# Kernel tuning notes

Measured on AMD Instinct MI355X. Metric: run time of the kernel, lower is better.

## Reference

```python
import jax, jax.numpy as jnp
import numpy as np

D_MODEL = 512
PROJ = 2 * D_MODEL  # 1024
N_STATES = 32
KSIZE = 4
LN_EPS = 1e-3  # keras LayerNormalization default epsilon


def setup_inputs() -> dict:
    key = jax.random.key(0)
    ks = jax.random.split(key, 16)
    B, L = 2, 2048
    s_in = 1.0 / np.sqrt(D_MODEL)
    s_pr = 1.0 / np.sqrt(PROJ)
    x = jax.random.normal(ks[0], (B, L, D_MODEL), dtype=jnp.float32)
    # LayerNorm params
    ln_gamma = jnp.ones((D_MODEL,), jnp.float32)
    ln_beta = jnp.zeros((D_MODEL,), jnp.float32)
    # dense1 / dense2: d_model -> proj
    W1 = jax.random.normal(ks[1], (D_MODEL, PROJ), jnp.float32) * s_in
    b1 = jnp.zeros((PROJ,), jnp.float32)
    W2 = jax.random.normal(ks[2], (D_MODEL, PROJ), jnp.float32) * s_in
    b2 = jnp.zeros((PROJ,), jnp.float32)
    # depthwise causal conv1d: kernel (K, 1, PROJ) in WIO layout, groups=PROJ
    conv_k = jax.random.normal(ks[3], (KSIZE, 1, PROJ), jnp.float32) * 0.5
    conv_b = jnp.zeros((PROJ,), jnp.float32)
    # SSM params
    A_log = jnp.log(jnp.broadcast_to(jnp.arange(1, N_STATES + 1, dtype=jnp.float32), (PROJ, N_STATES)))
    D_skip = jnp.ones((PROJ,), jnp.float32)
    WB = jax.random.normal(ks[4], (PROJ, N_STATES), jnp.float32) * s_pr
    bB = jnp.zeros((N_STATES,), jnp.float32)
    WC = jax.random.normal(ks[5], (PROJ, N_STATES), jnp.float32) * s_pr
    bC = jnp.zeros((N_STATES,), jnp.float32)
    Wd = jax.random.normal(ks[6], (PROJ, PROJ), jnp.float32) * s_pr
    bd = jnp.zeros((PROJ,), jnp.float32)
    # dense3: proj -> d_model
    W3 = jax.random.normal(ks[7], (PROJ, D_MODEL), jnp.float32) * s_pr
    b3 = jnp.zeros((D_MODEL,), jnp.float32)
    return dict(x=x, ln_gamma=ln_gamma, ln_beta=ln_beta, W1=W1, b1=b1, W2=W2, b2=b2,
                conv_k=conv_k, conv_b=conv_b, A_log=A_log, D_skip=D_skip,
                WB=WB, bB=bB, WC=WC, bC=bC, Wd=Wd, bd=bd, W3=W3, b3=b3)


def _layernorm(x, gamma, beta):
    mu = jnp.mean(x, axis=-1, keepdims=True)
    var = jnp.mean(jnp.square(x - mu), axis=-1, keepdims=True)
    return (x - mu) * jax.lax.rsqrt(var + LN_EPS) * gamma + beta


def _causal_dwconv(x, k, b):
    # x: [B,L,C], k: [K,1,C], depthwise causal conv (left-pad K-1)
    y = jax.lax.conv_general_dilated(
        x, k, window_strides=(1,), padding=[(KSIZE - 1, 0)],
        dimension_numbers=('NWC', 'WIO', 'NWC'), feature_group_count=PROJ)
    return y + b


def _selective_scan(u, delta, A, Bm, Cm, D_skip):
    # u, delta: [B,L,D]; A: [D,N]; Bm, Cm: [B,L,N]; D_skip: [D]
    deltaA = jnp.einsum('bld,dn->bldn', delta, A)                 # [B,L,D,N]
    deltaBu = jnp.einsum('bld,bld,bln->bldn', delta, u, Bm)        # [B,L,D,N]
    # shift deltaA left by one along L, zero at the end (pad trick in source)
    shifted = jnp.concatenate([deltaA[:, 1:], jnp.zeros_like(deltaA[:, :1])], axis=1)
    # reversed cumsum along L, then exp
    e = jnp.exp(jnp.flip(jnp.cumsum(jnp.flip(shifted, axis=1), axis=1), axis=1))
    xs = jnp.cumsum(deltaBu * e, axis=1) / (e + 1e-12)
    y = jnp.einsum('bldn,bln->bld', xs, Cm)
    return y + u * D_skip


def reference(x, ln_gamma, ln_beta, W1, b1, W2, b2, conv_k, conv_b,
              A_log, D_skip, WB, bB, WC, bC, Wd, bd, W3, b3):
    h = _layernorm(x, ln_gamma, ln_beta)
    x1 = h @ W1 + b1                      # [B,L,PROJ]
    x1 = _causal_dwconv(x1, conv_k, conv_b)
    x1 = jax.nn.silu(x1)
    A = -jnp.exp(A_log)                    # [PROJ,N]
    Cm = x1 @ WC + bC                      # [B,L,N]
    Bm = x1 @ WB + bB                      # [B,L,N]
    delta = jax.nn.softplus(x1 @ Wd + bd)  # [B,L,PROJ]
    y = _selective_scan(x1, delta, A, Bm, Cm, D_skip)
    x2 = jax.nn.silu(h @ W2 + b2)
    out = (y * x2) @ W3 + b3 + x           # residual; dropout is identity at inference
    return out
```

## Files before the change

kernel.cpp:

```cpp
#include <hip/hip_runtime.h>
#include <stdint.h>

#define L_SEQ 2048
#define BATCH 2
#define DMODEL 512
#define PROJ 1024
#define NST 32
#define NCAT 1152
#define ROWS (BATCH*L_SEQ)
#define THRESH 50.0f

typedef float f32x4 __attribute__((ext_vector_type(4)));
typedef short short8 __attribute__((ext_vector_type(8)));

__device__ inline float bf2f(unsigned short u){ uint32_t x=((uint32_t)u)<<16; float f; __builtin_memcpy(&f,&x,4); return f; }
__device__ inline unsigned short f2bf(float f){ uint32_t x; __builtin_memcpy(&x,&f,4); uint32_t r=x+0x7FFFu+((x>>16)&1u); return (unsigned short)(r>>16); }
__device__ inline float siluf(float x){ return x/(1.f+__expf(-x)); }
__device__ inline float softplusf(float x){ return x>20.f? x : log1pf(__expf(x)); }

#define AS1(p) ((const __attribute__((address_space(1))) void*)(p))
#define AS3(p) ((__attribute__((address_space(3))) void*)(p))

template<int N> __device__ inline void wait_vmcnt(){
  if constexpr (N==0)      asm volatile("s_waitcnt vmcnt(0)" ::: "memory");
  else if constexpr (N==1) asm volatile("s_waitcnt vmcnt(1)" ::: "memory");
  else if constexpr (N==2) asm volatile("s_waitcnt vmcnt(2)" ::: "memory");
  else if constexpr (N==3) asm volatile("s_waitcnt vmcnt(3)" ::: "memory");
  else if constexpr (N==4) asm volatile("s_waitcnt vmcnt(4)" ::: "memory");
  else if constexpr (N==5) asm volatile("s_waitcnt vmcnt(5)" ::: "memory");
  else if constexpr (N==6) asm volatile("s_waitcnt vmcnt(6)" ::: "memory");
  else                     asm volatile("s_waitcnt vmcnt(8)" ::: "memory");
}

__global__ __launch_bounds__(256)
void prep_kernel(const float* __restrict__ W1, const float* __restrict__ b1,
                 const float* __restrict__ W2, const float* __restrict__ b2,
                 const float* __restrict__ Wd, const float* __restrict__ bd,
                 const float* __restrict__ WB, const float* __restrict__ bB,
                 const float* __restrict__ WC, const float* __restrict__ bC,
                 const float* __restrict__ W3,
                 unsigned short* __restrict__ W12t, unsigned short* __restrict__ Wcatt,
                 unsigned short* __restrict__ W3t, float* __restrict__ bias12,
                 float* __restrict__ biascat)
{
  int i = blockIdx.x*256 + threadIdx.x;
  const int nA = 2048*512;
  const int nB = NCAT*1024;
  const int nC = 512*1024;
  if (i < nA) {
    int n = i >> 9, k = i & 511;
    float v = (n < 1024) ? W1[k*1024 + n] : W2[k*1024 + (n-1024)];
    W12t[i] = f2bf(v);
    return;
  }
  i -= nA;
  if (i < nB) {
    int n = i >> 10, k = i & 1023;
    float v;
    if (n < 1024) v = Wd[k*1024 + n];
    else if (n < 1056) v = WB[k*32 + (n-1024)];
    else if (n < 1088) v = WC[k*32 + (n-1056)];
    else v = 0.f;
    Wcatt[i] = f2bf(v);
    return;
  }
  i -= nB;
  if (i < nC) {
    int n = i >> 10, k = i & 1023;
    W3t[i] = f2bf(W3[k*512 + n]);
    return;
  }
  i -= nC;
  if (i < 2048) { bias12[i] = (i < 1024) ? b1[i] : b2[i-1024]; return; }
  i -= 2048;
  if (i < NCAT) {
    biascat[i] = (i < 1024) ? bd[i] : (i < 1056) ? bB[i-1024] : (i < 1088) ? bC[i-1056] : 0.f;
  }
}

__global__ __launch_bounds__(256)
void ln_kernel(const float* __restrict__ x, const float* __restrict__ gamma,
               const float* __restrict__ beta, unsigned short* __restrict__ H)
{
  int row = blockIdx.x*4 + (threadIdx.x >> 6);
  int lane = threadIdx.x & 63;
  const float4* xr = (const float4*)(x + (size_t)row*DMODEL);
  float4 v0 = xr[lane];
  float4 v1 = xr[lane+64];
  float s = v0.x+v0.y+v0.z+v0.w + v1.x+v1.y+v1.z+v1.w;
  float q = v0.x*v0.x+v0.y*v0.y+v0.z*v0.z+v0.w*v0.w
          + v1.x*v1.x+v1.y*v1.y+v1.z*v1.z+v1.w*v1.w;
#pragma unroll
  for (int m=32;m>0;m>>=1){ s += __shfl_xor(s,m); q += __shfl_xor(q,m); }
  float mu = s*(1.f/DMODEL);
  float var = q*(1.f/DMODEL) - mu*mu;
  float rs = rsqrtf(var + 1e-3f);
  int c0 = lane*4, c1 = 256 + lane*4;
  float4 g0 = *(const float4*)&gamma[c0]; float4 g1 = *(const float4*)&gamma[c1];
  float4 t0 = *(const float4*)&beta[c0];  float4 t1 = *(const float4*)&beta[c1];
  ushort4 o0, o1;
  o0.x = f2bf((v0.x-mu)*rs*g0.x + t0.x);
  o0.y = f2bf((v0.y-mu)*rs*g0.y + t0.y);
  o0.z = f2bf((v0.z-mu)*rs*g0.z + t0.z);
  o0.w = f2bf((v0.w-mu)*rs*g0.w + t0.w);
  o1.x = f2bf((v1.x-mu)*rs*g1.x + t1.x);
  o1.y = f2bf((v1.y-mu)*rs*g1.y + t1.y);
  o1.z = f2bf((v1.z-mu)*rs*g1.z + t1.z);
  o1.w = f2bf((v1.w-mu)*rs*g1.w + t1.w);
  *(ushort4*)&H[(size_t)row*DMODEL + c0] = o0;
  *(ushort4*)&H[(size_t)row*DMODEL + c1] = o1;
}

template<int BM, int BN, int WR, int WC, int MODE>
__global__ __launch_bounds__(256)
void gemm_bt(const unsigned short* __restrict__ A, const unsigned short* __restrict__ Bt,
             void* __restrict__ Cv, const float* __restrict__ bias,
             const float* __restrict__ res, int M, int N, int K)
{
  constexpr int BMW = BM/WR, BNW = BN/WC;
  constexpr int AM = BMW/16, AN = BNW/16;
  constexpr int ASEGI = BM*4/256;
  constexpr int BSEGI = BN*4/256;
  constexpr int LPT = ASEGI + BSEGI;
  __shared__ unsigned short As[3][BM*32];
  __shared__ unsigned short Bs[3][BN*32];
  int tid = threadIdx.x;
  int lane = tid & 63, wid = tid >> 6;
  int wm = wid / WC, wn = wid % WC;
  int m0 = blockIdx.x*BM, n0 = blockIdx.y*BN;

  f32x4 acc[AM][AN];
#pragma unroll
  for (int i=0;i<AM;i++)
#pragma unroll
    for (int j=0;j<AN;j++)
#pragma unroll
      for (int e=0;e<4;e++) acc[i][j][e] = 0.f;

  const unsigned short* ap[ASEGI];
  const unsigned short* bp[BSEGI];
#pragma unroll
  for (int j=0;j<ASEGI;j++){
    int s = tid + j*256;
    int row = s >> 2, kc = ((s & 3) ^ (row & 3)) * 8;
    ap[j] = A + (size_t)(m0+row)*K + kc;
  }
#pragma unroll
  for (int j=0;j<BSEGI;j++){
    int s = tid + j*256;
    int row = s >> 2, kc = ((s & 3) ^ (row & 3)) * 8;
    bp[j] = Bt + (size_t)(n0+row)*K + kc;
  }

  auto stage = [&](int buf){
#pragma unroll
    for (int j=0;j<ASEGI;j++){
      __builtin_amdgcn_global_load_lds(AS1(ap[j]), AS3(&As[buf][(size_t)(j*256 + wid*64)*8]), 16, 0, 0);
      ap[j] += 32;
    }
#pragma unroll
    for (int j=0;j<BSEGI;j++){
      __builtin_amdgcn_global_load_lds(AS1(bp[j]), AS3(&Bs[buf][(size_t)(j*256 + wid*64)*8]), 16, 0, 0);
      bp[j] += 32;
    }
  };

  stage(0);
  stage(1);
  int T = K/32;
  int rb = 0, wb = 2;
  int r = lane & 15, kb = lane >> 4;
  int kbx = kb ^ (r & 3);
  for (int t = 0; t < T; ++t) {
    if (t+1 < T) wait_vmcnt<LPT>();
    else         wait_vmcnt<0>();
    __builtin_amdgcn_s_barrier();
    if (t+2 < T) { stage(wb); wb = (wb==2)?0:wb+1; }
    short8 af[AM], bfr[AN];
#pragma unroll
    for (int i=0;i<AM;i++) af[i]  = *(const short8*)&As[rb][((wm*BMW + i*16 + r)*4 + kbx)*8];
#pragma unroll
    for (int j=0;j<AN;j++) bfr[j] = *(const short8*)&Bs[rb][((wn*BNW + j*16 + r)*4 + kbx)*8];
#pragma unroll
    for (int i=0;i<AM;i++)
#pragma unroll
      for (int j=0;j<AN;j++)
        acc[i][j] = __builtin_amdgcn_mfma_f32_16x16x32_bf16(af[i], bfr[j], acc[i][j], 0,0,0);
    rb = (rb==2)?0:rb+1;
  }

  int rr = (lane >> 4)*4, cc = lane & 15;
#pragma unroll
  for (int i=0;i<AM;i++)
#pragma unroll
    for (int j=0;j<AN;j++) {
      int col = n0 + wn*BNW + j*16 + cc;
      float bcol = (MODE == 4) ? 0.f : bias[col];
#pragma unroll
      for (int e=0;e<4;e++) {
        int row = m0 + wm*BMW + i*16 + rr + e;
        float v = acc[i][j][e];
        if constexpr (MODE == 4) {
          v += bias[row];
          if (row < 1024) v = softplusf(v);
          ((float*)Cv)[(size_t)row*N + col] = v;
        } else if constexpr (MODE == 0) {
          ((unsigned short*)Cv)[(size_t)row*N + col] = f2bf(v + bcol);
        } else if constexpr (MODE == 2) {
          v += bcol;
          if (col < 1024) v = softplusf(v);
          ((float*)Cv)[(size_t)row*N + col] = v;
        } else {
          v += bcol + res[(size_t)row*N + col];
          ((float*)Cv)[(size_t)row*N + col] = v;
        }
      }
    }
}

__global__ __launch_bounds__(256)
void conv_silu_kernel(const unsigned short* __restrict__ P12, const float* __restrict__ ck,
                      const float* __restrict__ cb, unsigned short* __restrict__ ubf,
                      unsigned short* __restrict__ x2bf)
{
  int gid = blockIdx.x*256 + threadIdx.x;
  int c4 = gid & 511;
  int row = gid >> 9;
  int l = row & (L_SEQ-1);
  if (c4 < 256) {
    int c = c4*4;
    float4 bv = *(const float4*)&cb[c];
    float r0=bv.x, r1=bv.y, r2=bv.z, r3=bv.w;
#pragma unroll
    for (int t=0;t<4;t++){
      int lsrc = l - 3 + t;
      if (lsrc >= 0) {
        ushort4 xv = *(const ushort4*)&P12[(size_t)(row-3+t)*2048 + c];
        float4 kv = *(const float4*)&ck[t*PROJ + c];
        r0 = fmaf(bf2f(xv.x),kv.x,r0);
        r1 = fmaf(bf2f(xv.y),kv.y,r1);
        r2 = fmaf(bf2f(xv.z),kv.z,r2);
        r3 = fmaf(bf2f(xv.w),kv.w,r3);
      }
    }
    ushort4 o;
    o.x=f2bf(siluf(r0)); o.y=f2bf(siluf(r1)); o.z=f2bf(siluf(r2)); o.w=f2bf(siluf(r3));
    *(ushort4*)&ubf[(size_t)row*PROJ + c] = o;
  } else {
    int c = (c4-256)*4;
    ushort4 xv = *(const ushort4*)&P12[(size_t)row*2048 + 1024 + c];
    ushort4 o;
    o.x=f2bf(siluf(bf2f(xv.x))); o.y=f2bf(siluf(bf2f(xv.y)));
    o.z=f2bf(siluf(bf2f(xv.z))); o.w=f2bf(siluf(bf2f(xv.w)));
    *(ushort4*)&x2bf[(size_t)row*PROJ + c] = o;
  }
}

__global__ __launch_bounds__(256)
void tsum_kernel(const float* __restrict__ CT, float* __restrict__ suf8,
                 int* __restrict__ l0out)
{
  int G = blockIdx.x;
  int b = G >> 10, d = G & 1023;
  const float* row = CT + (size_t)d*ROWS + b*L_SEQ;
  int t = threadIdx.x;
  float4 v0 = *(const float4*)&row[t*8];
  float4 v1 = *(const float4*)&row[t*8+4];
  float vals[8] = {v0.x,v0.y,v0.z,v0.w,v1.x,v1.y,v1.z,v1.w};
  float part = 0.f;
#pragma unroll
  for (int i=0;i<8;i++) part += vals[i];
  __shared__ float ps[256];
  ps[t] = part; __syncthreads();
  for (int off=1; off<256; off<<=1){
    float v = (t >= off) ? ps[t-off] : 0.f;
    __syncthreads();
    ps[t] += v;
    __syncthreads();
  }
  float T = ps[255];
  float prefx = ps[t] - part;
  suf8[(size_t)G*(L_SEQ/8) + t] = T - prefx;
  float run = prefx; int cnt = 0;
#pragma unroll
  for (int i=0;i<8;i++){
    float suf_l = T - run;
    cnt += (suf_l >= THRESH) ? 1 : 0;
    run += vals[i];
  }
  __shared__ int cs[256];
  cs[t] = cnt; __syncthreads();
  for (int off=128; off>0; off>>=1){ if (t < off) cs[t] += cs[t+off]; __syncthreads(); }
  if (t == 0) {
    int total = cs[0];
    l0out[G] = total > 0 ? total-1 : 0;
  }
}

__global__ __launch_bounds__(256)
void scan_kernel(const float* __restrict__ CT, const float* __restrict__ suf8,
                 const unsigned short* __restrict__ ubf, const float* __restrict__ A_log,
                 const int* __restrict__ l0arr, float* __restrict__ ystate)
{
  int tid = threadIdx.x;
  int n = tid & 31;
  int G = blockIdx.x*8 + (tid >> 5);
  int b = G >> 10, d = G & 1023;
  float np1 = __expf(A_log[d*NST + n]);
  int myl0 = l0arr[G];
  int base = min(myl0, __shfl_xor(myl0, 32)) & ~7;
  const float* dT = CT + (size_t)d*ROWS + b*L_SEQ;
  const float* Br = CT + (size_t)(1024+n)*ROWS + b*L_SEQ;
  const float* Cr = CT + (size_t)(1056+n)*ROWS + b*L_SEQ;
  const float* s8 = suf8 + (size_t)G*(L_SEQ/8);
  const unsigned short* ub = ubf + (size_t)b*L_SEQ*PROJ + d;
  float* yb = ystate + (size_t)b*L_SEQ*PROJ + d;
  float s = 0.f;
  for (int l = base; l < L_SEQ; l += 8) {
    float4 d0 = *(const float4*)&dT[l];
    float4 d1 = *(const float4*)&dT[l+4];
    float4 B0 = *(const float4*)&Br[l];
    float4 B1 = *(const float4*)&Br[l+4];
    float4 C0 = *(const float4*)&Cr[l];
    float4 C1 = *(const float4*)&Cr[l+4];
    float sufv = s8[l >> 3];
    float dl[8] = {d0.x,d0.y,d0.z,d0.w,d1.x,d1.y,d1.z,d1.w};
    float Bv[8] = {B0.x,B0.y,B0.z,B0.w,B1.x,B1.y,B1.z,B1.w};
    float Cv[8] = {C0.x,C0.y,C0.z,C0.w,C1.x,C1.y,C1.z,C1.w};
    float uu[8];
#pragma unroll
    for (int t=0;t<8;t++) uu[t] = bf2f(ub[(size_t)(l+t)*PROJ]);
    float cum = 0.f;
#pragma unroll
    for (int t=0;t<8;t++){
      cum += dl[t];
      float decay = __expf(-dl[t]*np1);
      s = fmaf(decay, s, dl[t]*uu[t]*Bv[t]);
      float gte = 1.f/(1.f + 1e-12f*__expf(np1*(sufv - cum)));
      float contrib = s*gte*Cv[t];
#pragma unroll
      for (int m=16;m>0;m>>=1) contrib += __shfl_xor(contrib, m);
      if (n == 0) yb[(size_t)(l+t)*PROJ] = contrib;
    }
  }
}

__global__ __launch_bounds__(256)
void zmul_kernel(const float* __restrict__ ystate, const unsigned short* __restrict__ ubf,
                 const unsigned short* __restrict__ x2bf, const float* __restrict__ Dskip,
                 const int* __restrict__ l0arr, unsigned short* __restrict__ zbf)
{
  size_t i = ((size_t)blockIdx.x*256 + threadIdx.x)*4;
  int d = (int)(i & (PROJ-1));
  int row = (int)(i >> 10);
  int l = row & (L_SEQ-1);
  int b = row >> 11;
  int4 l0v = *(const int4*)&l0arr[b*PROJ + d];
  float4 ys = *(const float4*)&ystate[i];
  ys.x = (l >= l0v.x) ? ys.x : 0.f;
  ys.y = (l >= l0v.y) ? ys.y : 0.f;
  ys.z = (l >= l0v.z) ? ys.z : 0.f;
  ys.w = (l >= l0v.w) ? ys.w : 0.f;
  ushort4 uu = *(const ushort4*)&ubf[i];
  ushort4 xx = *(const ushort4*)&x2bf[i];
  float4 Dv = *(const float4*)&Dskip[d];
  ushort4 o;
  o.x = f2bf((ys.x + bf2f(uu.x)*Dv.x)*bf2f(xx.x));
  o.y = f2bf((ys.y + bf2f(uu.y)*Dv.y)*bf2f(xx.y));
  o.z = f2bf((ys.z + bf2f(uu.z)*Dv.z)*bf2f(xx.z));
  o.w = f2bf((ys.w + bf2f(uu.w)*Dv.w)*bf2f(xx.w));
  *(ushort4*)&zbf[i] = o;
}

extern "C" void kernel_launch(void* const* d_in, const int* in_sizes, int n_in,
                              void* d_out, int out_size, void* d_ws, size_t ws_size,
                              hipStream_t stream)
{
  const float* x     = (const float*)d_in[0];
  const float* ln_g  = (const float*)d_in[1];
  const float* ln_b  = (const float*)d_in[2];
  const float* W1    = (const float*)d_in[3];
  const float* b1    = (const float*)d_in[4];
  const float* W2    = (const float*)d_in[5];
  const float* b2    = (const float*)d_in[6];
  const float* convk = (const float*)d_in[7];
  const float* convb = (const float*)d_in[8];
  const float* A_log = (const float*)d_in[9];
  const float* Dskip = (const float*)d_in[10];
  const float* WB    = (const float*)d_in[11];
  const float* bB    = (const float*)d_in[12];
  const float* WC    = (const float*)d_in[13];
  const float* bC    = (const float*)d_in[14];
  const float* Wd    = (const float*)d_in[15];
  const float* bd    = (const float*)d_in[16];
  const float* W3    = (const float*)d_in[17];
  const float* b3    = (const float*)d_in[18];

  char* w = (char*)d_ws;
  auto alloc = [&](size_t bytes){ char* p = w; w += (bytes + 255) & ~(size_t)255; return p; };
  unsigned short* Hbf    = (unsigned short*)alloc((size_t)ROWS*DMODEL*2);
  unsigned short* W12t   = (unsigned short*)alloc((size_t)2048*512*2);
  unsigned short* Wcatt  = (unsigned short*)alloc((size_t)NCAT*1024*2);
  unsigned short* W3t    = (unsigned short*)alloc((size_t)512*1024*2);
  float*          bias12 = (float*)alloc(2048*4);
  float*          biascat= (float*)alloc(NCAT*4);
  unsigned short* P12    = (unsigned short*)alloc((size_t)ROWS*2048*2);
  unsigned short* ubf    = (unsigned short*)alloc((size_t)ROWS*PROJ*2);
  unsigned short* x2bf   = (unsigned short*)alloc((size_t)ROWS*PROJ*2);
  float*          CT     = (float*)alloc((size_t)NCAT*ROWS*4);
  float*          suf8   = (float*)alloc((size_t)2048*(L_SEQ/8)*4);
  int*            l0arr  = (int*)alloc(2048*4);
  float*          ystate = (float*)alloc((size_t)ROWS*PROJ*4);
  unsigned short* zbf    = (unsigned short*)alloc((size_t)ROWS*PROJ*2);

  {
    int total = 2048*512 + NCAT*1024 + 512*1024 + 2048 + NCAT;
    prep_kernel<<<(total+255)/256, 256, 0, stream>>>(W1,b1,W2,b2,Wd,bd,WB,bB,WC,bC,W3,
                                                     W12t,Wcatt,W3t,bias12,biascat);
  }
  ln_kernel<<<ROWS/4, 256, 0, stream>>>(x, ln_g, ln_b, Hbf);

  dim3 g1(ROWS/64, 2048/64);
  gemm_bt<64,64,2,2,0><<<g1, 256, 0, stream>>>(Hbf, W12t, P12, bias12, nullptr, ROWS, 2048, DMODEL);

  conv_silu_kernel<<<ROWS*512/256, 256, 0, stream>>>(P12, convk, convb, ubf, x2bf);

  dim3 g2(NCAT/64, ROWS/64);
  gemm_bt<64,64,2,2,4><<<g2, 256, 0, stream>>>(Wcatt, ubf, CT, biascat, nullptr, NCAT, ROWS, PROJ);

  tsum_kernel<<<2048, 256, 0, stream>>>(CT, suf8, l0arr);

  scan_kernel<<<2048/8, 256, 0, stream>>>(CT, suf8, ubf, A_log, l0arr, ystate);

  zmul_kernel<<<(ROWS*PROJ/4)/256, 256, 0, stream>>>(ystate, ubf, x2bf, Dskip, l0arr, zbf);

  dim3 g3(ROWS/64, DMODEL/64);
  gemm_bt<64,64,2,2,3><<<g3, 256, 0, stream>>>(zbf, W3t, (float*)d_out, b3, x, ROWS, DMODEL, PROJ);
}
```

Measured before the change: 162.6 us.

## Double GEMM K-tile, add XCD-aware block remap, trim concatenated padding

The bf16 MFMA GEMM now stages K tiles of 64 instead of 32, with an 8-way XOR swizzle. This halves the number of barrier and wait iterations per output tile. Workgroup IDs are also remapped so that consecutive blocks in the same XCD round-robin slot cover contiguous output tiles, aiming at better L2 reuse. The concatenated delta/B/C weight matrix drops from 1152 to 1088 rows, which removes zero-padding work from that GEMM and from the CT buffer. The cost is double the LDS per stage, and the remap assumes the block count is divisible by 8.

```diff
diff --git a/kernel.cpp b/kernel.cpp
--- a/kernel.cpp
+++ b/kernel.cpp
@@ -6,7 +6,7 @@
 #define DMODEL 512
 #define PROJ 1024
 #define NST 32
-#define NCAT 1152
+#define NCATU 1088
 #define ROWS (BATCH*L_SEQ)
 #define THRESH 50.0f
 
@@ -23,11 +23,8 @@
 
 template<int N> __device__ inline void wait_vmcnt(){
   if constexpr (N==0)      asm volatile("s_waitcnt vmcnt(0)" ::: "memory");
-  else if constexpr (N==1) asm volatile("s_waitcnt vmcnt(1)" ::: "memory");
   else if constexpr (N==2) asm volatile("s_waitcnt vmcnt(2)" ::: "memory");
-  else if constexpr (N==3) asm volatile("s_waitcnt vmcnt(3)" ::: "memory");
   else if constexpr (N==4) asm volatile("s_waitcnt vmcnt(4)" ::: "memory");
-  else if constexpr (N==5) asm volatile("s_waitcnt vmcnt(5)" ::: "memory");
   else if constexpr (N==6) asm volatile("s_waitcnt vmcnt(6)" ::: "memory");
   else                     asm volatile("s_waitcnt vmcnt(8)" ::: "memory");
 }
@@ -45,7 +42,7 @@
 {
   int i = blockIdx.x*256 + threadIdx.x;
   const int nA = 2048*512;
-  const int nB = NCAT*1024;
+  const int nB = NCATU*1024;
   const int nC = 512*1024;
   if (i < nA) {
     int n = i >> 9, k = i & 511;
@@ -59,8 +56,7 @@
     float v;
     if (n < 1024) v = Wd[k*1024 + n];
     else if (n < 1056) v = WB[k*32 + (n-1024)];
-    else if (n < 1088) v = WC[k*32 + (n-1056)];
-    else v = 0.f;
+    else v = WC[k*32 + (n-1056)];
     Wcatt[i] = f2bf(v);
     return;
   }
@@ -73,8 +69,8 @@
   i -= nC;
   if (i < 2048) { bias12[i] = (i < 1024) ? b1[i] : b2[i-1024]; return; }
   i -= 2048;
-  if (i < NCAT) {
-    biascat[i] = (i < 1024) ? bd[i] : (i < 1056) ? bB[i-1024] : (i < 1088) ? bC[i-1056] : 0.f;
+  if (i < NCATU) {
+    biascat[i] = (i < 1024) ? bd[i] : (i < 1056) ? bB[i-1024] : bC[i-1056];
   }
 }
 
@@ -111,23 +107,29 @@
   *(ushort4*)&H[(size_t)row*DMODEL + c1] = o1;
 }
 
-template<int BM, int BN, int WR, int WC, int MODE>
+template<int BM, int BN, int MODE>
 __global__ __launch_bounds__(256)
 void gemm_bt(const unsigned short* __restrict__ A, const unsigned short* __restrict__ Bt,
              void* __restrict__ Cv, const float* __restrict__ bias,
              const float* __restrict__ res, int M, int N, int K)
 {
-  constexpr int BMW = BM/WR, BNW = BN/WC;
-  constexpr int AM = BMW/16, AN = BNW/16;
-  constexpr int ASEGI = BM*4/256;
-  constexpr int BSEGI = BN*4/256;
+  constexpr int BK = 64;
+  constexpr int AM = 2, AN = 2;
+  constexpr int ASEGI = BM*BK/8/256;
+  constexpr int BSEGI = BN*BK/8/256;
   constexpr int LPT = ASEGI + BSEGI;
-  __shared__ unsigned short As[3][BM*32];
-  __shared__ unsigned short Bs[3][BN*32];
+  __shared__ unsigned short As[3][BM*BK];
+  __shared__ unsigned short Bs[3][BN*BK];
   int tid = threadIdx.x;
   int lane = tid & 63, wid = tid >> 6;
-  int wm = wid / WC, wn = wid % WC;
-  int m0 = blockIdx.x*BM, n0 = blockIdx.y*BN;
+  int wm = wid >> 1, wn = wid & 1;
+
+  int gx = gridDim.x;
+  int nwg = gx * gridDim.y;
+  int L = blockIdx.y*gx + blockIdx.x;
+  int W = (L & 7)*(nwg >> 3) + (L >> 3);
+  int bx = W % gx, by = W / gx;
+  int m0 = bx*BM, n0 = by*BN;
 
   f32x4 acc[AM][AN];
 #pragma unroll
@@ -142,13 +144,13 @@
 #pragma unroll
   for (int j=0;j<ASEGI;j++){
     int s = tid + j*256;
-    int row = s >> 2, kc = ((s & 3) ^ (row & 3)) * 8;
+    int row = s >> 3, kc = ((s & 7) ^ (row & 7)) * 8;
     ap[j] = A + (size_t)(m0+row)*K + kc;
   }
 #pragma unroll
   for (int j=0;j<BSEGI;j++){
     int s = tid + j*256;
-    int row = s >> 2, kc = ((s & 3) ^ (row & 3)) * 8;
+    int row = s >> 3, kc = ((s & 7) ^ (row & 7)) * 8;
     bp[j] = Bt + (size_t)(n0+row)*K + kc;
   }
 
@@ -156,36 +158,46 @@
 #pragma unroll
     for (int j=0;j<ASEGI;j++){
       __builtin_amdgcn_global_load_lds(AS1(ap[j]), AS3(&As[buf][(size_t)(j*256 + wid*64)*8]), 16, 0, 0);
-      ap[j] += 32;
+      ap[j] += BK;
     }
 #pragma unroll
     for (int j=0;j<BSEGI;j++){
       __builtin_amdgcn_global_load_lds(AS1(bp[j]), AS3(&Bs[buf][(size_t)(j*256 + wid*64)*8]), 16, 0, 0);
-      bp[j] += 32;
+      bp[j] += BK;
     }
   };
 
   stage(0);
   stage(1);
-  int T = K/32;
+  int T = K/BK;
   int rb = 0, wb = 2;
   int r = lane & 15, kb = lane >> 4;
-  int kbx = kb ^ (r & 3);
   for (int t = 0; t < T; ++t) {
     if (t+1 < T) wait_vmcnt<LPT>();
     else         wait_vmcnt<0>();
     __builtin_amdgcn_s_barrier();
     if (t+2 < T) { stage(wb); wb = (wb==2)?0:wb+1; }
-    short8 af[AM], bfr[AN];
-#pragma unroll
-    for (int i=0;i<AM;i++) af[i]  = *(const short8*)&As[rb][((wm*BMW + i*16 + r)*4 + kbx)*8];
-#pragma unroll
-    for (int j=0;j<AN;j++) bfr[j] = *(const short8*)&Bs[rb][((wn*BNW + j*16 + r)*4 + kbx)*8];
-#pragma unroll
-    for (int i=0;i<AM;i++)
-#pragma unroll
-      for (int j=0;j<AN;j++)
-        acc[i][j] = __builtin_amdgcn_mfma_f32_16x16x32_bf16(af[i], bfr[j], acc[i][j], 0,0,0);
+#pragma unroll
+    for (int ks=0; ks<2; ++ks) {
+      short8 af[AM], bfr[AN];
+#pragma unroll
+      for (int i=0;i<AM;i++){
+        int row = wm*32 + i*16 + r;
+        int c = (ks*4 + kb) ^ (r & 7);
+        af[i] = *(const short8*)&As[rb][(row*8 + c)*8];
+      }
+#pragma unroll
+      for (int j=0;j<AN;j++){
+        int row = wn*32 + j*16 + r;
+        int c = (ks*4 + kb) ^ (r & 7);
+        bfr[j] = *(const short8*)&Bs[rb][(row*8 + c)*8];
+      }
+#pragma unroll
+      for (int i=0;i<AM;i++)
+#pragma unroll
+        for (int j=0;j<AN;j++)
+          acc[i][j] = __builtin_amdgcn_mfma_f32_16x16x32_bf16(af[i], bfr[j], acc[i][j], 0,0,0);
+    }
     rb = (rb==2)?0:rb+1;
   }
 
@@ -194,11 +206,11 @@
   for (int i=0;i<AM;i++)
 #pragma unroll
     for (int j=0;j<AN;j++) {
-      int col = n0 + wn*BNW + j*16 + cc;
+      int col = n0 + wn*32 + j*16 + cc;
       float bcol = (MODE == 4) ? 0.f : bias[col];
 #pragma unroll
       for (int e=0;e<4;e++) {
-        int row = m0 + wm*BMW + i*16 + rr + e;
+        int row = m0 + wm*32 + i*16 + rr + e;
         float v = acc[i][j][e];
         if constexpr (MODE == 4) {
           v += bias[row];
@@ -206,10 +218,6 @@
           ((float*)Cv)[(size_t)row*N + col] = v;
         } else if constexpr (MODE == 0) {
           ((unsigned short*)Cv)[(size_t)row*N + col] = f2bf(v + bcol);
-        } else if constexpr (MODE == 2) {
-          v += bcol;
-          if (col < 1024) v = softplusf(v);
-          ((float*)Cv)[(size_t)row*N + col] = v;
         } else {
           v += bcol + res[(size_t)row*N + col];
           ((float*)Cv)[(size_t)row*N + col] = v;
@@ -400,33 +408,33 @@
   auto alloc = [&](size_t bytes){ char* p = w; w += (bytes + 255) & ~(size_t)255; return p; };
   unsigned short* Hbf    = (unsigned short*)alloc((size_t)ROWS*DMODEL*2);
   unsigned short* W12t   = (unsigned short*)alloc((size_t)2048*512*2);
-  unsigned short* Wcatt  = (unsigned short*)alloc((size_t)NCAT*1024*2);
+  unsigned short* Wcatt  = (unsigned short*)alloc((size_t)NCATU*1024*2);
   unsigned short* W3t    = (unsigned short*)alloc((size_t)512*1024*2);
   float*          bias12 = (float*)alloc(2048*4);
-  float*          biascat= (float*)alloc(NCAT*4);
+  float*          biascat= (float*)alloc(NCATU*4);
   unsigned short* P12    = (unsigned short*)alloc((size_t)ROWS*2048*2);
   unsigned short* ubf    = (unsigned short*)alloc((size_t)ROWS*PROJ*2);
   unsigned short* x2bf   = (unsigned short*)alloc((size_t)ROWS*PROJ*2);
-  float*          CT     = (float*)alloc((size_t)NCAT*ROWS*4);
+  float*          CT     = (float*)alloc((size_t)NCATU*ROWS*4);
   float*          suf8   = (float*)alloc((size_t)2048*(L_SEQ/8)*4);
   int*            l0arr  = (int*)alloc(2048*4);
   float*          ystate = (float*)alloc((size_t)ROWS*PROJ*4);
   unsigned short* zbf    = (unsigned short*)alloc((size_t)ROWS*PROJ*2);
 
   {
-    int total = 2048*512 + NCAT*1024 + 512*1024 + 2048 + NCAT;
+    int total = 2048*512 + NCATU*1024 + 512*1024 + 2048 + NCATU;
     prep_kernel<<<(total+255)/256, 256, 0, stream>>>(W1,b1,W2,b2,Wd,bd,WB,bB,WC,bC,W3,
                                                      W12t,Wcatt,W3t,bias12,biascat);
   }
   ln_kernel<<<ROWS/4, 256, 0, stream>>>(x, ln_g, ln_b, Hbf);
 
   dim3 g1(ROWS/64, 2048/64);
-  gemm_bt<64,64,2,2,0><<<g1, 256, 0, stream>>>(Hbf, W12t, P12, bias12, nullptr, ROWS, 2048, DMODEL);
+  gemm_bt<64,64,0><<<g1, 256, 0, stream>>>(Hbf, W12t, P12, bias12, nullptr, ROWS, 2048, DMODEL);
 
   conv_silu_kernel<<<ROWS*512/256, 256, 0, stream>>>(P12, convk, convb, ubf, x2bf);
 
-  dim3 g2(NCAT/64, ROWS/64);
-  gemm_bt<64,64,2,2,4><<<g2, 256, 0, stream>>>(Wcatt, ubf, CT, biascat, nullptr, NCAT, ROWS, PROJ);
+  dim3 g2(NCATU/64, ROWS/64);
+  gemm_bt<64,64,4><<<g2, 256, 0, stream>>>(Wcatt, ubf, CT, biascat, nullptr, NCATU, ROWS, PROJ);
 
   tsum_kernel<<<2048, 256, 0, stream>>>(CT, suf8, l0arr);
 
@@ -435,5 +443,5 @@
   zmul_kernel<<<(ROWS*PROJ/4)/256, 256, 0, stream>>>(ystate, ubf, x2bf, Dskip, l0arr, zbf);
 
   dim3 g3(ROWS/64, DMODEL/64);
-  gemm_bt<64,64,2,2,3><<<g3, 256, 0, stream>>>(zbf, W3t, (float*)d_out, b3, x, ROWS, DMODEL, PROJ);
-}
+  gemm_bt<64,64,3><<<g3, 256, 0, stream>>>(zbf, W3t, (float*)d_out, b3, x, ROWS, DMODEL, PROJ);
+}
```

New measurement: 160.2 us. No clear change (-1.5%).
